# Kernel optimization log

Hardware: AMD Instinct MI355X
Metric: run time of the kernel (lower is better)

## Reference

```python
import jax, jax.numpy as jnp
import numpy as np

# --- constants from the source module ---
VS = 10.0          # voltage scale: state stores v/VS
GS = 100.0         # leak conductance scale (g_l / GS used in _i_l)
TAYLOR_EPS = 0.1   # switch to Taylor expansion near removable singularity
HH_GATE_EPS = 1e-5 # clip gates away from {0,1}
DT = 0.02          # HMM observation interval (ode integrated 0 -> DT)
N_STEPS = 10       # multi_step_euler: ConstantStepSize with dt0 = DT/10
# Huys & Paninski / standard HH channel parameters
G_NA, E_NA = 120.0, 50.0
G_K,  E_K  = 36.0, -77.0
G_L,  E_L  = 30.0, -54.387
C_M = 1.0


def _safe_ratio(v, shift):
    # x / (1 - exp(-x/10)) with first-order Taylor (10 + 0.5*x) near x=0.
    # Source uses lax.cond on jnp.any(|x|<eps); elementwise where is the
    # faithful vectorized form for batched states.
    x = v + shift
    exact = x / (1.0 - jnp.exp(-x / 10.0))
    taylor = 10.0 + 0.5 * x
    return jnp.where(jnp.abs(x) < TAYLOR_EPS, taylor, exact)


def _alpha_m(v): return 0.1 * _safe_ratio(v, 35.0)
def _beta_m(v):  return 4.0 * jnp.exp(-(v + 65.0) / 18.0)
def _alpha_n(v): return 0.01 * _safe_ratio(v, 55.0)
def _beta_n(v):  return 0.125 * jnp.exp(-(v + 65.0) / 80.0)
def _alpha_h(v): return 0.07 * jnp.exp(-(v + 50.0) / 20.0)
def _beta_h(v):  return 1.0 / (jnp.exp(-(v + 35.0) / 10.0) + 1.0)


def _vector_field(state, i_ext):
    # state: [B, 4*C] laid out as [v/VS | logit(n) | logit(m) | logit(h)]
    v_s, ln, lm, lh = jnp.split(state, 4, axis=-1)
    v = VS * v_s  # membrane potential in mV, [B, C]
    n = jnp.clip(jax.nn.sigmoid(ln), HH_GATE_EPS, 1.0 - HH_GATE_EPS)
    m = jnp.clip(jax.nn.sigmoid(lm), HH_GATE_EPS, 1.0 - HH_GATE_EPS)
    h = jnp.clip(jax.nn.sigmoid(lh), HH_GATE_EPS, 1.0 - HH_GATE_EPS)

    i_na = G_NA * m**3 * h * (v - E_NA)
    i_k = G_K * n**4 * (v - E_K)
    i_l = (G_L / GS) * (v - E_L)
    dv_s = (i_ext - i_na - i_k - i_l) / (C_M * VS)

    dn = _alpha_n(v) * (1.0 - n) - _beta_n(v) * n
    dm = _alpha_m(v) * (1.0 - m) - _beta_m(v) * m
    dh = _alpha_h(v) * (1.0 - h) - _beta_h(v) * h
    # chain rule into logit space: d logit(x)/dt = dx/dt / (x (1 - x))
    dln = dn / (n * (1.0 - n))
    dlm = dm / (m * (1.0 - m))
    dlh = dh / (h * (1.0 - h))
    return jnp.concatenate([dv_s, dln, dlm, dlh], axis=-1)


def setup_inputs() -> dict:
    key = jax.random.key(0)
    k1, k2, k3 = jax.random.split(key, 3)
    B, C = 32768, 128
    # v near resting potential (-65 mV -> -6.5 in scaled units), gate logits ~ N(0,1)
    v0 = -6.5 + 0.3 * jax.random.normal(k1, (B, C), dtype=jnp.float32)
    gates = jax.random.normal(k2, (B, 3 * C), dtype=jnp.float32)
    state = jnp.concatenate([v0, gates], axis=-1)  # [B, 4C]
    i_ext = 10.0 * jax.random.uniform(k3, (C,), dtype=jnp.float32)
    return {"state": state, "i_ext": i_ext}


def reference(state, i_ext):
    # multi-step Euler: 10 constant steps of DT/10 from t0=0 to t1=DT
    h = DT / N_STEPS

    def step(s, _):
        return s + h * _vector_field(s, i_ext), None

    out, _ = jax.lax.scan(step, state, None, length=N_STEPS)
    return out
```

## Files before the change

### kernel.cpp

```cpp
#include <hip/hip_runtime.h>
#include <stdint.h>

#define LOG2E    1.4426950408889634f
#define NLN2     -0.6931471805599453f
#define NL720    -0.0020037431123457824f
#define QB       -0.07013100893210239f
#define EM2      0.13533528323661270f
#define BN_C     0.08592215f
#define AH_C     0.03306561f
#define BM_C     0.75550365f
#define HSTEP    0.002f
#define HLOG     -0.0028853900817779268f

__device__ __forceinline__ float bf2f(uint32_t lo16) {
  union { uint32_t u; float f; } c; c.u = lo16 << 16; return c.f;
}

__device__ __forceinline__ void unpack8(uint4 u, float* f) {
  f[0] = bf2f(u.x & 0xffffu); f[1] = bf2f(u.x >> 16);
  f[2] = bf2f(u.y & 0xffffu); f[3] = bf2f(u.y >> 16);
  f[4] = bf2f(u.z & 0xffffu); f[5] = bf2f(u.z >> 16);
  f[6] = bf2f(u.w & 0xffffu); f[7] = bf2f(u.w >> 16);
}

__device__ __forceinline__ void load8(const void* p, int elem_off, bool is_f32,
                                      float* f) {
  if (is_f32) {
    const float4* q = (const float4*)((const float*)p + elem_off);
    float4 a = q[0], b = q[1];
    f[0] = a.x; f[1] = a.y; f[2] = a.z; f[3] = a.w;
    f[4] = b.x; f[5] = b.y; f[6] = b.z; f[7] = b.w;
  } else {
    unpack8(*(const uint4*)((const unsigned short*)p + elem_off), f);
  }
}

__device__ __forceinline__ void store8f(float* p, const float* f) {
  *(float4*)(p)     = make_float4(f[0], f[1], f[2], f[3]);
  *(float4*)(p + 4) = make_float4(f[4], f[5], f[6], f[7]);
}

__global__ __launch_bounds__(256) void hh_kernel(
    const void* __restrict__ state,
    const void* __restrict__ iext,
    float* __restrict__ out,
    int C, int ngroups , int nthreads) {
  __shared__ uint32_t sflags[2];
  if (threadIdx.x < 64) {
    uint32_t wi = ((const uint32_t*)iext)[threadIdx.x];
    unsigned long long bi = __ballot((wi & 0x8000u) != 0u);
    uint32_t ws = ((const uint32_t*)state)[threadIdx.x & 31];
    unsigned long long bs = __ballot(((ws >> 7) & 0xFFu) != 0x81u);
    if (threadIdx.x == 0) {
      sflags[0] = bs ? 1u : 0u;
      sflags[1] = bi ? 1u : 0u;
    }
  }
  __syncthreads();
  bool s_f32 = sflags[0] != 0u;
  bool i_f32 = sflags[1] != 0u;

  int g = blockIdx.x * blockDim.x + threadIdx.x;
  if (g >= nthreads) return;
  int b  = g / ngroups;
  int gc = g - b * ngroups;
  int base = b * 4 * C + gc * 8;

  float v[8], ln[8], lm[8], lh[8], ie[8];
  load8(state, base,         s_f32, v);
  load8(state, base + C,     s_f32, ln);
  load8(state, base + 2 * C, s_f32, lm);
  load8(state, base + 3 * C, s_f32, lh);
  load8(iext,  gc * 8,       i_f32, ie);
#pragma unroll
  for (int i = 0; i < 8; ++i) {
    v[i]  *= 10.0f;
    ln[i] *= -LOG2E;
    lm[i] *= -LOG2E;
    lh[i] *= -LOG2E;
  }

#pragma unroll 1
  for (int s = 0; s < 10; ++s) {
#pragma unroll
    for (int i = 0; i < 8; ++i) {
      float en = __builtin_amdgcn_exp2f(ln[i]);
      float em = __builtin_amdgcn_exp2f(lm[i]);
      float eh = __builtin_amdgcn_exp2f(lh[i]);
      float qq = __builtin_amdgcn_exp2f(__builtin_fmaf(v[i], NL720, QB));

      float q2 = qq * qq, q4 = q2 * q2, q8 = q4 * q4, q9 = q8 * qq;
      float q18 = q9 * q9, q36 = q18 * q18, q40 = q36 * q4, q72 = q36 * q36;
      float e1 = q72;
      float e2 = q72 * EM2;
      float bn = BN_C * q9;
      float ah = AH_C * q36;
      float bm = BM_C * q40;

      float x1 = v[i] + 35.0f;
      float x2 = v[i] + 55.0f;
      bool  t1 = fabsf(x1) < 0.1f;
      bool  t2 = fabsf(x2) < 0.1f;

      float d1 = 1.0f + en, d2 = 1.0f + em, d3 = 1.0f + eh;
      float d7 = t1 ? 1.0f : (1.0f - e1);
      float d8 = t2 ? 1.0f : (1.0f - e2);
      float f6 = (1.0f + e1) * eh;

      float p2 = d1 * d2, p3 = p2 * d3, p4 = p3 * en;
      float p5 = p4 * em, p6 = p5 * f6, p7 = p6 * d7, p8 = p7 * d8;
      float r  = __builtin_amdgcn_rcpf(p8);
      float ian_ = r * p7;  r *= d8;
      float iam_ = r * p6;  r *= d7;
      float i9e  = r * p5;  r *= f6;
      float iem  = r * p4;  r *= em;
      float ien  = r * p3;  r *= en;
      float hg   = r * p2;  r *= d3;
      float m    = r * d1;  r *= d2;
      float n    = r;

      float m3h = m * m * m * hg;
      float n4  = n * n; n4 *= n4;
      float dv  = ie[i];
      dv = __builtin_fmaf(-120.0f, m3h * (v[i] - 50.0f), dv);
      dv = __builtin_fmaf(-36.0f,  n4  * (v[i] + 77.0f), dv);
      dv = __builtin_fmaf(-0.3f,   v[i] + 54.387f,       dv);

      float am = t1 ? __builtin_fmaf(0.05f, x1, 1.0f)  : 0.1f  * (x1 * iam_);
      float an = t2 ? __builtin_fmaf(0.005f, x2, 0.1f) : 0.01f * (x2 * ian_);

      float dln = d1 * __builtin_fmaf(-bn, ien, an);
      float dlm = d2 * __builtin_fmaf(-bm, iem, am);
      float dlh = d3 * (ah - i9e);

      v[i]  = __builtin_fmaf(HSTEP, dv,  v[i]);
      ln[i] = __builtin_fmaf(HLOG,  dln, ln[i]);
      lm[i] = __builtin_fmaf(HLOG,  dlm, lm[i]);
      lh[i] = __builtin_fmaf(HLOG,  dlh, lh[i]);
    }
  }

#pragma unroll
  for (int i = 0; i < 8; ++i) {
    v[i]  *= 0.1f;
    ln[i] *= NLN2;
    lm[i] *= NLN2;
    lh[i] *= NLN2;
  }
  store8f(out + base,         v);
  store8f(out + base + C,     ln);
  store8f(out + base + 2 * C, lm);
  store8f(out + base + 3 * C, lh);
}

extern "C" void kernel_launch(void* const* d_in, const int* in_sizes, int n_in,
                              void* d_out, int out_size, void* d_ws, size_t ws_size,
                              hipStream_t stream) {
  const void* state = d_in[0];
  const void* iext  = d_in[1];
  float* out = (float*)d_out;

  int C = in_sizes[1];
  int cells = in_sizes[0] / 4;
  int nthreads = cells / 8;
  int ngroups = C / 8;
  int block = 256;
  int grid = (nthreads + block - 1) / block;
  hh_kernel<<<grid, block, 0, stream>>>(state, iext, out, C, ngroups, nthreads);
}
```

Baseline: 152.7 us.

## Process two row halves per thread, prefetching the second during compute

Each thread now handles two 8-cell groups, one from each half of the batch. The second group's raw input is loaded into registers before the first group's ten Euler steps run, so its memory latency is hidden behind compute. Outputs are written with nontemporal stores, and the per-step constant arithmetic is folded away: the leak constant moves into a pre-adjusted i_ext, and the Taylor-branch variables are rescaled to save an add and a multiply. The changes also set a launch-bounds occupancy hint, halve the grid, and raise register pressure from the prefetch buffer.

```diff
diff --git a/kernel.cpp b/kernel.cpp
--- a/kernel.cpp
+++ b/kernel.cpp
@@ -11,6 +11,9 @@
 #define BM_C     0.75550365f
 #define HSTEP    0.002f
 #define HLOG     -0.0028853900817779268f
+#define IE_ADJ   16.3161f
+
+typedef float cf4 __attribute__((ext_vector_type(4)));
 
 __device__ __forceinline__ float bf2f(uint32_t lo16) {
   union { uint32_t u; float f; } c; c.u = lo16 << 16; return c.f;
@@ -35,43 +38,14 @@
   }
 }
 
-__device__ __forceinline__ void store8f(float* p, const float* f) {
-  *(float4*)(p)     = make_float4(f[0], f[1], f[2], f[3]);
-  *(float4*)(p + 4) = make_float4(f[4], f[5], f[6], f[7]);
-}
-
-__global__ __launch_bounds__(256) void hh_kernel(
-    const void* __restrict__ state,
-    const void* __restrict__ iext,
-    float* __restrict__ out,
-    int C, int ngroups , int nthreads) {
-  __shared__ uint32_t sflags[2];
-  if (threadIdx.x < 64) {
-    uint32_t wi = ((const uint32_t*)iext)[threadIdx.x];
-    unsigned long long bi = __ballot((wi & 0x8000u) != 0u);
-    uint32_t ws = ((const uint32_t*)state)[threadIdx.x & 31];
-    unsigned long long bs = __ballot(((ws >> 7) & 0xFFu) != 0x81u);
-    if (threadIdx.x == 0) {
-      sflags[0] = bs ? 1u : 0u;
-      sflags[1] = bi ? 1u : 0u;
-    }
-  }
-  __syncthreads();
-  bool s_f32 = sflags[0] != 0u;
-  bool i_f32 = sflags[1] != 0u;
-
-  int g = blockIdx.x * blockDim.x + threadIdx.x;
-  if (g >= nthreads) return;
-  int b  = g / ngroups;
-  int gc = g - b * ngroups;
-  int base = b * 4 * C + gc * 8;
-
-  float v[8], ln[8], lm[8], lh[8], ie[8];
-  load8(state, base,         s_f32, v);
-  load8(state, base + C,     s_f32, ln);
-  load8(state, base + 2 * C, s_f32, lm);
-  load8(state, base + 3 * C, s_f32, lh);
-  load8(iext,  gc * 8,       i_f32, ie);
+__device__ __forceinline__ void store8f_nt(float* p, const float* f) {
+  cf4 a = {f[0], f[1], f[2], f[3]};
+  cf4 b = {f[4], f[5], f[6], f[7]};
+  __builtin_nontemporal_store(a, (cf4*)p);
+  __builtin_nontemporal_store(b, (cf4*)(p + 4));
+}
+
+__device__ __forceinline__ void scale_in(float* v, float* ln, float* lm, float* lh) {
 #pragma unroll
   for (int i = 0; i < 8; ++i) {
     v[i]  *= 10.0f;
@@ -79,7 +53,20 @@
     lm[i] *= -LOG2E;
     lh[i] *= -LOG2E;
   }
-
+}
+
+__device__ __forceinline__ void scale_out(float* v, float* ln, float* lm, float* lh) {
+#pragma unroll
+  for (int i = 0; i < 8; ++i) {
+    v[i]  *= 0.1f;
+    ln[i] *= NLN2;
+    lm[i] *= NLN2;
+    lh[i] *= NLN2;
+  }
+}
+
+__device__ __forceinline__ void hh10(float* v, float* ln, float* lm, float* lh,
+                                     const float* iep) {
 #pragma unroll 1
   for (int s = 0; s < 10; ++s) {
 #pragma unroll
@@ -97,10 +84,10 @@
       float ah = AH_C * q36;
       float bm = BM_C * q40;
 
-      float x1 = v[i] + 35.0f;
-      float x2 = v[i] + 55.0f;
-      bool  t1 = fabsf(x1) < 0.1f;
-      bool  t2 = fabsf(x2) < 0.1f;
+      float x1 = __builtin_fmaf(0.1f,  v[i], 3.5f);
+      float x2 = __builtin_fmaf(0.01f, v[i], 0.55f);
+      bool  t1 = fabsf(x1) < 0.01f;
+      bool  t2 = fabsf(x2) < 0.001f;
 
       float d1 = 1.0f + en, d2 = 1.0f + em, d3 = 1.0f + eh;
       float d7 = t1 ? 1.0f : (1.0f - e1);
@@ -121,13 +108,12 @@
 
       float m3h = m * m * m * hg;
       float n4  = n * n; n4 *= n4;
-      float dv  = ie[i];
+      float dv  = __builtin_fmaf(-0.3f, v[i], iep[i]);
       dv = __builtin_fmaf(-120.0f, m3h * (v[i] - 50.0f), dv);
       dv = __builtin_fmaf(-36.0f,  n4  * (v[i] + 77.0f), dv);
-      dv = __builtin_fmaf(-0.3f,   v[i] + 54.387f,       dv);
-
-      float am = t1 ? __builtin_fmaf(0.05f, x1, 1.0f)  : 0.1f  * (x1 * iam_);
-      float an = t2 ? __builtin_fmaf(0.005f, x2, 0.1f) : 0.01f * (x2 * ian_);
+
+      float am = t1 ? __builtin_fmaf(0.5f, x1, 1.0f) : x1 * iam_;
+      float an = t2 ? __builtin_fmaf(0.5f, x2, 0.1f) : x2 * ian_;
 
       float dln = d1 * __builtin_fmaf(-bn, ien, an);
       float dlm = d2 * __builtin_fmaf(-bm, iem, am);
@@ -139,18 +125,101 @@
       lh[i] = __builtin_fmaf(HLOG,  dlh, lh[i]);
     }
   }
-
-#pragma unroll
-  for (int i = 0; i < 8; ++i) {
-    v[i]  *= 0.1f;
-    ln[i] *= NLN2;
-    lm[i] *= NLN2;
-    lh[i] *= NLN2;
-  }
-  store8f(out + base,         v);
-  store8f(out + base + C,     ln);
-  store8f(out + base + 2 * C, lm);
-  store8f(out + base + 3 * C, lh);
+}
+
+template <bool SF32>
+__device__ __forceinline__ void run_both(const void* __restrict__ state,
+                                         float* __restrict__ out,
+                                         const float* iep,
+                                         int base0, int base1, bool has2,
+                                         int C) {
+  float v[8], ln[8], lm[8], lh[8];
+  load8(state, base0,         SF32, v);
+  load8(state, base0 + C,     SF32, ln);
+  load8(state, base0 + 2 * C, SF32, lm);
+  load8(state, base0 + 3 * C, SF32, lh);
+
+  uint4 rb[SF32 ? 8 : 4];
+  if (has2) {
+    if constexpr (SF32) {
+      const float* sp = (const float*)state;
+#pragma unroll
+      for (int k = 0; k < 4; ++k) {
+        rb[2 * k]     = *(const uint4*)(sp + base1 + k * C);
+        rb[2 * k + 1] = *(const uint4*)(sp + base1 + k * C + 4);
+      }
+    } else {
+      const unsigned short* sp = (const unsigned short*)state;
+#pragma unroll
+      for (int k = 0; k < 4; ++k)
+        rb[k] = *(const uint4*)(sp + base1 + k * C);
+    }
+  }
+
+  scale_in(v, ln, lm, lh);
+  hh10(v, ln, lm, lh, iep);
+  scale_out(v, ln, lm, lh);
+  store8f_nt(out + base0,         v);
+  store8f_nt(out + base0 + C,     ln);
+  store8f_nt(out + base0 + 2 * C, lm);
+  store8f_nt(out + base0 + 3 * C, lh);
+
+  if (has2) {
+    if constexpr (SF32) {
+      const float* fb = (const float*)rb;
+#pragma unroll
+      for (int i = 0; i < 8; ++i) {
+        v[i] = fb[i]; ln[i] = fb[8 + i]; lm[i] = fb[16 + i]; lh[i] = fb[24 + i];
+      }
+    } else {
+      unpack8(rb[0], v); unpack8(rb[1], ln);
+      unpack8(rb[2], lm); unpack8(rb[3], lh);
+    }
+    scale_in(v, ln, lm, lh);
+    hh10(v, ln, lm, lh, iep);
+    scale_out(v, ln, lm, lh);
+    store8f_nt(out + base1,         v);
+    store8f_nt(out + base1 + C,     ln);
+    store8f_nt(out + base1 + 2 * C, lm);
+    store8f_nt(out + base1 + 3 * C, lh);
+  }
+}
+
+__global__ __launch_bounds__(256, 4) void hh_kernel(
+    const void* __restrict__ state,
+    const void* __restrict__ iext,
+    float* __restrict__ out,
+    int C, int ngroups , int nfirst, int nsecond, int half_elems) {
+  __shared__ uint32_t sflags[2];
+  if (threadIdx.x < 64) {
+    uint32_t wi = ((const uint32_t*)iext)[threadIdx.x];
+    unsigned long long bi = __ballot((wi & 0x8000u) != 0u);
+    uint32_t ws = ((const uint32_t*)state)[threadIdx.x & 31];
+    unsigned long long bs = __ballot(((ws >> 7) & 0xFFu) != 0x81u);
+    if (threadIdx.x == 0) {
+      sflags[0] = bs ? 1u : 0u;
+      sflags[1] = bi ? 1u : 0u;
+    }
+  }
+  __syncthreads();
+  bool s_f32 = sflags[0] != 0u;
+  bool i_f32 = sflags[1] != 0u;
+
+  int g = blockIdx.x * blockDim.x + threadIdx.x;
+  if (g >= nfirst) return;
+  int b  = g / ngroups;
+  int gc = g - b * ngroups;
+  int base0 = b * 4 * C + gc * 8;
+  int base1 = base0 + half_elems;
+  bool has2 = g < nsecond;
+
+  float ie[8], iep[8];
+  load8(iext, gc * 8, i_f32, ie);
+#pragma unroll
+  for (int i = 0; i < 8; ++i) iep[i] = ie[i] - IE_ADJ;
+
+  if (s_f32) run_both<true >(state, out, iep, base0, base1, has2, C);
+  else       run_both<false>(state, out, iep, base0, base1, has2, C);
 }
 
 extern "C" void kernel_launch(void* const* d_in, const int* in_sizes, int n_in,
@@ -162,9 +231,14 @@
 
   int C = in_sizes[1];
   int cells = in_sizes[0] / 4;
-  int nthreads = cells / 8;
+  int Brows = cells / C;
   int ngroups = C / 8;
+  int B0 = (Brows + 1) / 2;
+  int nfirst  = B0 * ngroups;
+  int nsecond = (Brows - B0) * ngroups;
+  int half_elems = B0 * 4 * C;
   int block = 256;
-  int grid = (nthreads + block - 1) / block;
-  hh_kernel<<<grid, block, 0, stream>>>(state, iext, out, C, ngroups, nthreads);
-}
+  int grid = (nfirst + block - 1) / block;
+  hh_kernel<<<grid, block, 0, stream>>>(state, iext, out, C, ngroups,
+                                        nfirst, nsecond, half_elems);
+}
```

Result: slower. 173.5 us (+13.7%).
